# Performance work log

Hardware: AMD Instinct MI355X
Metric: run time of the kernel (lower is better)

## Reference

```python
import jax, jax.numpy as jnp
import numpy as np

N = 1_000_000   # active voxels
CIN = 32
COUT = 64
K = 9           # 3x3 kernel offsets (rulebook size)
EPS = 1e-5


def setup_inputs() -> dict:
    key = jax.random.key(0)
    ks = jax.random.split(key, 6)
    x = jax.random.normal(ks[0], (N, CIN), dtype=jnp.float32)
    # rulebook: neighbor index per (voxel, kernel offset); stride=1 so same coord set
    nbr = jax.random.randint(ks[1], (N, K), 0, N, dtype=jnp.int32)
    W1 = jax.random.normal(ks[2], (K, CIN, COUT), dtype=jnp.float32) * (1.0 / np.sqrt(K * CIN))
    W2 = jax.random.normal(ks[3], (K, COUT, COUT), dtype=jnp.float32) * (1.0 / np.sqrt(K * COUT))
    Wd = jax.random.normal(ks[4], (CIN, COUT), dtype=jnp.float32) * (1.0 / np.sqrt(CIN))
    g1 = jnp.ones((COUT,), jnp.float32); b1 = jnp.zeros((COUT,), jnp.float32)
    g2 = jnp.ones((COUT,), jnp.float32); b2 = jnp.zeros((COUT,), jnp.float32)
    gd = jnp.ones((COUT,), jnp.float32); bd = jnp.zeros((COUT,), jnp.float32)
    return {"x": x, "W1": W1, "g1": g1, "b1": b1, "W2": W2, "g2": g2, "b2": b2,
            "Wd": Wd, "gd": gd, "bd": bd, "nbr": nbr}


def _sparse_conv(x, nbr, W):
    # gather-GEMM-scatter; loop over the fixed K=9 kernel offsets to avoid
    # materializing the full [N, K, Cin] gathered tensor
    out = jnp.zeros((x.shape[0], W.shape[-1]), dtype=x.dtype)
    for k in range(W.shape[0]):
        out = out + jnp.take(x, nbr[:, k], axis=0) @ W[k]
    return out


def _bn(x, gamma, beta):
    # BatchNorm1d over the voxel dimension (training-mode batch statistics)
    mu = jnp.mean(x, axis=0)
    var = jnp.var(x, axis=0)
    return gamma * (x - mu) * jax.lax.rsqrt(var + EPS) + beta


def reference(x, W1, g1, b1, W2, g2, b2, Wd, gd, bd, nbr):
    # downsample branch (1x1 conv -> BN, no relu) since in_ch != out_ch
    identity = _bn(x @ Wd, gd, bd)
    # conv1: SparseConv3x3 -> BN -> ReLU
    out = jax.nn.relu(_bn(_sparse_conv(x, nbr, W1), g1, b1))
    # conv2: SparseConv3x3 -> BN (no relu)
    out = _bn(_sparse_conv(out, nbr, W2), g2, b2)
    # residual add + final ReLU
    return jax.nn.relu(out + identity)
```

## Files before the change

### kernel.cpp

```cpp
#include <hip/hip_runtime.h>
#include <hip/hip_bf16.h>

#define NV 1000000
#define CI 32
#define CO 64
#define KK 9
#define NG (NV / 16)
#define EPSV 1e-5f

typedef __bf16 bf16x8 __attribute__((ext_vector_type(8)));
typedef float  f32x4  __attribute__((ext_vector_type(4)));

__device__ __forceinline__ f32x4 mfma16(bf16x8 a, bf16x8 b, f32x4 c) {
    return __builtin_amdgcn_mfma_f32_16x16x32_bf16(a, b, c, 0, 0, 0);
}

__device__ __forceinline__ float xredseg(float v) {
    v += __shfl_xor(v, 16, 64);
    v += __shfl_xor(v, 32, 64);
    return v;
}

__global__ void k_prep_w(const float* __restrict__ W1, const float* __restrict__ W2,
                         const float* __restrict__ Wd,
                         __bf16* __restrict__ W1T, __bf16* __restrict__ W2T,
                         __bf16* __restrict__ WdT) {
    int i = blockIdx.x * blockDim.x + threadIdx.x;
    const int n1 = KK * CO * CI;
    const int n2 = KK * CO * CO;
    const int nd = CO * CI;
    if (i < n1) {
        int k = i / (CO * CI), r = i % (CO * CI), co = r / CI, ci = r % CI;
        W1T[i] = (__bf16)W1[(k * CI + ci) * CO + co];
    } else if (i < n1 + n2) {
        int j = i - n1;
        int k = j / (CO * CO), r = j % (CO * CO), co = r / CO, ci = r % CO;
        W2T[j] = (__bf16)W2[(k * CO + ci) * CO + co];
    } else if (i < n1 + n2 + nd) {
        int j = i - n1 - n2;
        int co = j / CI, ci = j % CI;
        WdT[j] = (__bf16)Wd[ci * CO + co];
    }
}

__global__ void k_prep_x(const float* __restrict__ x, __bf16* __restrict__ xb) {
    int i = blockIdx.x * blockDim.x + threadIdx.x;
    const float4* px = (const float4*)x + 2 * (size_t)i;
    float4 u = px[0], v = px[1];
    bf16x8 o;
    o[0] = (__bf16)u.x; o[1] = (__bf16)u.y; o[2] = (__bf16)u.z; o[3] = (__bf16)u.w;
    o[4] = (__bf16)v.x; o[5] = (__bf16)v.y; o[6] = (__bf16)v.z; o[7] = (__bf16)v.w;
    *((bf16x8*)xb + i) = o;
}

__global__ __launch_bounds__(256, 2) void k_conv1(
    const __bf16* __restrict__ xb, const int* __restrict__ nbr,
    const __bf16* __restrict__ W1T, const __bf16* __restrict__ WdT,
    __bf16* __restrict__ y1b, float* __restrict__ stats) {
    __shared__ __align__(16) char w1smem[KK * CO * CI * 2];

    const int lane = threadIdx.x & 63;
    const int w    = threadIdx.x >> 6;
    const int r    = lane & 15;
    const int seg  = lane >> 4;
    const int sseg = seg ^ ((r >> 1) & 3);

#pragma unroll
    for (int j = 0; j < 9; j++) {
        int c    = j * 256 + threadIdx.x;
        int segc = c & 3;
        int rc   = (c >> 2) & 15;
        int csrc = (c & ~3) | (segc ^ ((rc >> 1) & 3));
        const __bf16* srcp = W1T + (size_t)csrc * 8;
        __builtin_amdgcn_global_load_lds(
            (const __attribute__((address_space(1))) void*)srcp,
            (__attribute__((address_space(3))) void*)(w1smem + j * 4096 + w * 1024),
            16, 0, 0);
    }
    __syncthreads();

    bf16x8 wd[4];
#pragma unroll
    for (int t = 0; t < 4; t++)
        wd[t] = *(const bf16x8*)(WdT + (size_t)(t * 16 + r) * CI + seg * 8);

    float ps1[4] = {0.f,0.f,0.f,0.f}, pq1[4] = {0.f,0.f,0.f,0.f};
    float psd[4] = {0.f,0.f,0.f,0.f}, pqd[4] = {0.f,0.f,0.f,0.f};

    const int slot   = blockIdx.x * 4 + w;
    const int stride = gridDim.x * 4;
    const f32x4 z = {0.f, 0.f, 0.f, 0.f};

    auto loadIdx = [&](int (&idx)[KK], int tile) {
        const int* nb = nbr + (size_t)(tile * 16 + r) * KK;
#pragma unroll
        for (int k = 0; k < KK; k++) idx[k] = nb[k];
    };
    auto gather9 = [&](bf16x8 (&g)[KK], const int (&idx)[KK]) {
#pragma unroll
        for (int k = 0; k < KK; k++)
            g[k] = *(const bf16x8*)(xb + (size_t)idx[k] * CI + seg * 8);
    };
    auto loadAd = [&](int tile) {
        return *(const bf16x8*)(xb + (size_t)(tile * 16 + r) * CI + seg * 8);
    };
    auto compute = [&](int tile, const bf16x8 (&g)[KK], bf16x8 ad) {
        int w1off = 0;
        asm volatile("" : "+v"(w1off));
        const __bf16* wb = (const __bf16*)w1smem + w1off;

        f32x4 acc[4]  = {z, z, z, z};
        f32x4 accd[4] = {z, z, z, z};
#pragma unroll
        for (int t = 0; t < 4; t++) accd[t] = mfma16(ad, wd[t], accd[t]);
#pragma unroll
        for (int k = 0; k < KK; k++) {
#pragma unroll
            for (int t = 0; t < 4; t++) {
                bf16x8 b = *(const bf16x8*)(wb + k * 2048 + t * 512 + r * 32 + sseg * 8);
                acc[t] = mfma16(g[k], b, acc[t]);
            }
        }

        const int vb = tile * 16;
#pragma unroll
        for (int t = 0; t < 4; t++) {
#pragma unroll
            for (int rr = 0; rr < 4; rr++) {
                float val = acc[t][rr];
                int row = vb + seg * 4 + rr;
                __builtin_nontemporal_store((__bf16)val, &y1b[(size_t)row * CO + t * 16 + r]);
                ps1[t] += val; pq1[t] += val * val;
                float dv = accd[t][rr];
                psd[t] += dv; pqd[t] += dv * dv;
            }
        }
    };

    int idx0[KK], idx1[KK];
    bf16x8 g0[KK], g1[KK];
    bf16x8 ad0, ad1;

    int it = slot;
    loadIdx(idx0, it);
    gather9(g0, idx0); ad0 = loadAd(it);
    int itn = it + stride;
    bool have = (itn < NG);
    if (have) loadIdx(idx1, itn);

    while (true) {
        if (have) {
            gather9(g1, idx1); ad1 = loadAd(itn);
            int it2 = itn + stride;
            if (it2 < NG) loadIdx(idx0, it2);
        }
        compute(it, g0, ad0);
        if (!have) break;
        it = itn; itn = it + stride; have = (itn < NG);

        if (have) {
            gather9(g0, idx0); ad0 = loadAd(itn);
            int it2 = itn + stride;
            if (it2 < NG) loadIdx(idx1, it2);
        }
        compute(it, g1, ad1);
        if (!have) break;
        it = itn; itn = it + stride; have = (itn < NG);
    }

#pragma unroll
    for (int t = 0; t < 4; t++) {
        ps1[t] = xredseg(ps1[t]); pq1[t] = xredseg(pq1[t]);
        psd[t] = xredseg(psd[t]); pqd[t] = xredseg(pqd[t]);
    }
    if (lane < 16) {
#pragma unroll
        for (int t = 0; t < 4; t++) {
            atomicAdd(&stats[0 * 64 + t * 16 + lane], ps1[t]);
            atomicAdd(&stats[1 * 64 + t * 16 + lane], pq1[t]);
            atomicAdd(&stats[2 * 64 + t * 16 + lane], psd[t]);
            atomicAdd(&stats[3 * 64 + t * 16 + lane], pqd[t]);
        }
    }
}

#define TILE_B (16 * KK * 128)

__global__ __launch_bounds__(128, 2) void k_conv2(
    const __bf16* __restrict__ h1b, const int* __restrict__ nbr,
    const __bf16* __restrict__ W2T, const float* __restrict__ g1,
    const float* __restrict__ b1,
    float* __restrict__ y2, float* __restrict__ stats) {
    __shared__ __align__(16) char smem[2][TILE_B];

    const int lane = threadIdx.x & 63;
    const int w    = threadIdx.x >> 6;
    const int r    = lane & 15;
    const int seg  = lane >> 4;
    const int p    = lane & 7;

    bf16x8 w2[KK][2][2];
#pragma unroll
    for (int k = 0; k < KK; k++)
#pragma unroll
        for (int t2 = 0; t2 < 2; t2++)
#pragma unroll
            for (int s = 0; s < 2; s++) {
                int co = w * 32 + t2 * 16 + r;
                int ci = s * 32 + seg * 8;
                w2[k][t2][s] = *(const bf16x8*)(W2T + ((size_t)(k * CO + co)) * CO + ci);
            }

    float scP[8], shP[8];
#pragma unroll
    for (int j = 0; j < 8; j++) {
        int c0 = p * 8 + j;
        float mu  = stats[c0] * (1.0f / NV);
        float var = stats[64 + c0] * (1.0f / NV) - mu * mu;
        float s   = g1[c0] * rsqrtf(var + EPSV);
        scP[j] = s; shP[j] = b1[c0] - mu * s;
    }

    int ri[9], dstoff[9];
#pragma unroll
    for (int s = 0; s < 9; s++) {
        int c = w * 576 + s * 64 + lane;
        int rIdx = c >> 3;
        int i = (rIdx * 57) >> 9;
        ri[s] = rIdx;
        dstoff[s] = rIdx * 128 + ((p ^ (i & 7)) * 16);
    }

    auto loadIdx = [&](int (&ix)[9], int tile) {
        const int* nb = nbr + (size_t)tile * (16 * KK);
#pragma unroll
        for (int s = 0; s < 9; s++) ix[s] = nb[ri[s]];
    };
    auto loadDat = [&](f32x4 (&d)[9], const int (&ix)[9]) {
#pragma unroll
        for (int s = 0; s < 9; s++)
            d[s] = *(const f32x4*)(h1b + (size_t)ix[s] * CO + p * 8);
    };
    auto xform = [&](char* tb, const f32x4 (&d)[9]) {
#pragma unroll
        for (int s = 0; s < 9; s++) {
            union { f32x4 f; bf16x8 b; } u; u.f = d[s];
            bf16x8 o;
#pragma unroll
            for (int j = 0; j < 8; j++)
                o[j] = (__bf16)fmaxf((float)u.b[j] * scP[j] + shP[j], 0.f);
            *(bf16x8*)(tb + dstoff[s]) = o;
        }
    };

    float ps[2] = {0.f, 0.f}, pq[2] = {0.f, 0.f};
    const f32x4 z = {0.f, 0.f, 0.f, 0.f};
    const int sw = r & 7;
    const int G = gridDim.x;

    int idxN[9]; f32x4 dat[9];
    int it = blockIdx.x;
    loadIdx(idxN, it);
    loadDat(dat, idxN);
    { int t1 = it + G;     loadIdx(idxN, t1 < NG ? t1 : NG - 1); }
    xform(smem[0], dat);
    loadDat(dat, idxN);
    { int t2 = it + 2 * G; loadIdx(idxN, t2 < NG ? t2 : NG - 1); }
    __syncthreads();
    int cur = 0;

    for (; it < NG; it += G) {
        const __bf16* base = (const __bf16*)smem[cur];
        f32x4 acc[2] = {z, z};
#pragma unroll
        for (int k = 0; k < KK; k++) {
            const __bf16* rp = base + (size_t)(r * KK + k) * 64;
            bf16x8 a0 = *(const bf16x8*)(rp + ((seg ^ sw) * 8));
            bf16x8 a1 = *(const bf16x8*)(rp + (((4 + seg) ^ sw) * 8));
            acc[0] = mfma16(a0, w2[k][0][0], acc[0]);
            acc[0] = mfma16(a1, w2[k][0][1], acc[0]);
            acc[1] = mfma16(a0, w2[k][1][0], acc[1]);
            acc[1] = mfma16(a1, w2[k][1][1], acc[1]);
        }

        const int vb = it * 16;
#pragma unroll
        for (int t2 = 0; t2 < 2; t2++) {
#pragma unroll
            for (int rr = 0; rr < 4; rr++) {
                float val = acc[t2][rr];
                int row = vb + seg * 4 + rr;
                int c = w * 32 + t2 * 16 + r;
                __builtin_nontemporal_store(val, &y2[(size_t)row * CO + c]);
                ps[t2] += val; pq[t2] += val * val;
            }
        }

        int nx = it + G;
        if (nx < NG) {
            xform(smem[cur ^ 1], dat);
            loadDat(dat, idxN);
            { int t3 = it + 3 * G; loadIdx(idxN, t3 < NG ? t3 : NG - 1); }
            __syncthreads();
            cur ^= 1;
        }
    }

#pragma unroll
    for (int t2 = 0; t2 < 2; t2++) { ps[t2] = xredseg(ps[t2]); pq[t2] = xredseg(pq[t2]); }
    if (lane < 16) {
#pragma unroll
        for (int t2 = 0; t2 < 2; t2++) {
            atomicAdd(&stats[4 * 64 + w * 32 + t2 * 16 + lane], ps[t2]);
            atomicAdd(&stats[5 * 64 + w * 32 + t2 * 16 + lane], pq[t2]);
        }
    }
}

__global__ __launch_bounds__(256, 2) void k_final(
    const __bf16* __restrict__ xb, const __bf16* __restrict__ WdT,
    float* __restrict__ out, const float* __restrict__ stats,
    const float* __restrict__ g2, const float* __restrict__ b2,
    const float* __restrict__ gd, const float* __restrict__ bd) {
    __shared__ float s2[CO], sh2[CO], sdv[CO], shd[CO];
    int t = threadIdx.x;
    if (t < CO) {
        float mu2  = stats[4 * 64 + t] * (1.0f / NV);
        float var2 = stats[5 * 64 + t] * (1.0f / NV) - mu2 * mu2;
        float s = g2[t] * rsqrtf(var2 + EPSV);
        s2[t] = s; sh2[t] = b2[t] - mu2 * s;
        float mud  = stats[2 * 64 + t] * (1.0f / NV);
        float vard = stats[3 * 64 + t] * (1.0f / NV) - mud * mud;
        float sd = gd[t] * rsqrtf(vard + EPSV);
        sdv[t] = sd; shd[t] = bd[t] - mud * sd;
    }
    __syncthreads();

    const int lane = threadIdx.x & 63;
    const int w    = threadIdx.x >> 6;
    const int r    = lane & 15;
    const int seg  = lane >> 4;

    bf16x8 wd[4];
#pragma unroll
    for (int t4 = 0; t4 < 4; t4++)
        wd[t4] = *(const bf16x8*)(WdT + (size_t)(t4 * 16 + r) * CI + seg * 8);

    const int slot = blockIdx.x * 4 + w;
    const int nslots = gridDim.x * 4;
    const f32x4 z = {0.f, 0.f, 0.f, 0.f};

    for (int gid = slot; gid < NG; gid += nslots) {
        const int vb = gid * 16;
        const int v  = vb + r;
        bf16x8 ad = *(const bf16x8*)(xb + (size_t)v * CI + seg * 8);
        f32x4 accd[4] = {z, z, z, z};
#pragma unroll
        for (int t4 = 0; t4 < 4; t4++) accd[t4] = mfma16(ad, wd[t4], accd[t4]);
#pragma unroll
        for (int t4 = 0; t4 < 4; t4++) {
#pragma unroll
            for (int rr = 0; rr < 4; rr++) {
                int row = vb + seg * 4 + rr;
                int c = t4 * 16 + r;
                size_t o = (size_t)row * CO + c;
                float y2v = out[o];
                float res = s2[c] * y2v + sh2[c] + sdv[c] * accd[t4][rr] + shd[c];
                out[o] = fmaxf(res, 0.f);
            }
        }
    }
}

extern "C" void kernel_launch(void* const* d_in, const int* in_sizes, int n_in,
                              void* d_out, int out_size, void* d_ws, size_t ws_size,
                              hipStream_t stream) {
    const float* x  = (const float*)d_in[0];
    const float* W1 = (const float*)d_in[1];
    const float* g1 = (const float*)d_in[2];
    const float* b1 = (const float*)d_in[3];
    const float* W2 = (const float*)d_in[4];
    const float* g2 = (const float*)d_in[5];
    const float* b2 = (const float*)d_in[6];
    const float* Wd = (const float*)d_in[7];
    const float* gd = (const float*)d_in[8];
    const float* bd = (const float*)d_in[9];
    const int*  nbr = (const int*)d_in[10];

    char* ws = (char*)d_ws;
    __bf16* xb  = (__bf16*)ws;
    __bf16* y1b = (__bf16*)(ws + 64000000);
    __bf16* W1T = (__bf16*)(ws + 192000000);
    __bf16* W2T = W1T + KK * CO * CI;
    __bf16* WdT = W2T + KK * CO * CO;
    float* stats = (float*)(ws + 192000000 + 2 * (KK*CO*CI + KK*CO*CO + CO*CI));

    hipMemsetAsync(stats, 0, 6 * 64 * sizeof(float), stream);

    int nprep = KK*CO*CI + KK*CO*CO + CO*CI;
    k_prep_w<<<(nprep + 255) / 256, 256, 0, stream>>>(W1, W2, Wd, W1T, W2T, WdT);
    k_prep_x<<<(NV * CI / 8) / 256, 256, 0, stream>>>(x, xb);
    k_conv1<<<768, 256, 0, stream>>>(xb, nbr, W1T, WdT, y1b, stats);
    k_conv2<<<1024, 128, 0, stream>>>(y1b, nbr, W2T, g1, b1, (float*)d_out, stats);
    k_final<<<1024, 256, 0, stream>>>(xb, WdT, (float*)d_out, stats, g2, b2, gd, bd);
}
```

Before: 601.5 us.

## Stage conv outputs through LDS for wide stores and keep conv2 output in bf16

conv1 now writes its bf16 tile into a swizzled per-wave LDS buffer and then stores 16-byte vectors, instead of scattering 2-byte nontemporal stores. When the workspace is large enough, conv2 does the same and keeps its output as a bf16 intermediate, so the final kernel reads half the bytes and writes the fp32 output with nontemporal stores. This cuts write and readback traffic for the intermediates. It adds LDS usage and an extra rounding of the pre-BN conv2 output to bf16, and the bf16 path depends on the workspace size.

```diff
diff --git a/kernel.cpp b/kernel.cpp
--- a/kernel.cpp
+++ b/kernel.cpp
@@ -9,6 +9,7 @@
 #define EPSV 1e-5f
 
 typedef __bf16 bf16x8 __attribute__((ext_vector_type(8)));
+typedef __bf16 bf16x4 __attribute__((ext_vector_type(4)));
 typedef float  f32x4  __attribute__((ext_vector_type(4)));
 
 __device__ __forceinline__ f32x4 mfma16(bf16x8 a, bf16x8 b, f32x4 c) {
@@ -58,6 +59,7 @@
     const __bf16* __restrict__ W1T, const __bf16* __restrict__ WdT,
     __bf16* __restrict__ y1b, float* __restrict__ stats) {
     __shared__ __align__(16) char w1smem[KK * CO * CI * 2];
+    __shared__ __align__(16) char ystage[4][2048];
 
     const int lane = threadIdx.x & 63;
     const int w    = threadIdx.x >> 6;
@@ -123,17 +125,28 @@
         }
 
         const int vb = tile * 16;
+        char* yst = ystage[w];
 #pragma unroll
         for (int t = 0; t < 4; t++) {
 #pragma unroll
             for (int rr = 0; rr < 4; rr++) {
                 float val = acc[t][rr];
-                int row = vb + seg * 4 + rr;
-                __builtin_nontemporal_store((__bf16)val, &y1b[(size_t)row * CO + t * 16 + r]);
                 ps1[t] += val; pq1[t] += val * val;
                 float dv = accd[t][rr];
                 psd[t] += dv; pqd[t] += dv * dv;
-            }
+                int row = seg * 4 + rr;
+                int byte = row * 128 + ((t * 32 + 2 * r) ^ ((row & 7) << 4));
+                *(__bf16*)(yst + byte) = (__bf16)val;
+            }
+        }
+#pragma unroll
+        for (int q = 0; q < 2; q++) {
+            int c    = lane * 2 + q;
+            int row  = c >> 3;
+            int part = c & 7;
+            bf16x8 v = *(const bf16x8*)(yst + row * 128 + ((part ^ (row & 7)) << 4));
+            __builtin_nontemporal_store(
+                v, (bf16x8*)(y1b + (size_t)vb * CO + (size_t)c * 8));
         }
     };
 
@@ -186,12 +199,15 @@
 
 #define TILE_B (16 * KK * 128)
 
+template <bool BF16OUT>
 __global__ __launch_bounds__(128, 2) void k_conv2(
     const __bf16* __restrict__ h1b, const int* __restrict__ nbr,
     const __bf16* __restrict__ W2T, const float* __restrict__ g1,
     const float* __restrict__ b1,
-    float* __restrict__ y2, float* __restrict__ stats) {
+    __bf16* __restrict__ y2b, float* __restrict__ y2f,
+    float* __restrict__ stats) {
     __shared__ __align__(16) char smem[2][TILE_B];
+    __shared__ __align__(16) char ystage2[2][1024];
 
     const int lane = threadIdx.x & 63;
     const int w    = threadIdx.x >> 6;
@@ -284,15 +300,37 @@
         }
 
         const int vb = it * 16;
-#pragma unroll
-        for (int t2 = 0; t2 < 2; t2++) {
-#pragma unroll
-            for (int rr = 0; rr < 4; rr++) {
-                float val = acc[t2][rr];
-                int row = vb + seg * 4 + rr;
-                int c = w * 32 + t2 * 16 + r;
-                __builtin_nontemporal_store(val, &y2[(size_t)row * CO + c]);
-                ps[t2] += val; pq[t2] += val * val;
+        if constexpr (BF16OUT) {
+            char* yst = ystage2[w];
+#pragma unroll
+            for (int t2 = 0; t2 < 2; t2++) {
+#pragma unroll
+                for (int rr = 0; rr < 4; rr++) {
+                    float val = acc[t2][rr];
+                    ps[t2] += val; pq[t2] += val * val;
+                    int row = seg * 4 + rr;
+                    int byte = row * 64 + ((t2 * 32 + 2 * r) ^ ((row >> 2) << 4));
+                    *(__bf16*)(yst + byte) = (__bf16)val;
+                }
+            }
+            {
+                int row  = lane >> 2;
+                int part = lane & 3;
+                bf16x8 v = *(const bf16x8*)(yst + row * 64 + ((part ^ (row >> 2)) << 4));
+                __builtin_nontemporal_store(
+                    v, (bf16x8*)(y2b + (size_t)(vb + row) * CO + w * 32 + part * 8));
+            }
+        } else {
+#pragma unroll
+            for (int t2 = 0; t2 < 2; t2++) {
+#pragma unroll
+                for (int rr = 0; rr < 4; rr++) {
+                    float val = acc[t2][rr];
+                    int row = vb + seg * 4 + rr;
+                    int c = w * 32 + t2 * 16 + r;
+                    __builtin_nontemporal_store(val, &y2f[(size_t)row * CO + c]);
+                    ps[t2] += val; pq[t2] += val * val;
+                }
             }
         }
 
@@ -317,8 +355,10 @@
     }
 }
 
+template <bool BF16IN>
 __global__ __launch_bounds__(256, 2) void k_final(
     const __bf16* __restrict__ xb, const __bf16* __restrict__ WdT,
+    const __bf16* __restrict__ y2b,
     float* __restrict__ out, const float* __restrict__ stats,
     const float* __restrict__ g2, const float* __restrict__ b2,
     const float* __restrict__ gd, const float* __restrict__ bd) {
@@ -364,9 +404,11 @@
                 int row = vb + seg * 4 + rr;
                 int c = t4 * 16 + r;
                 size_t o = (size_t)row * CO + c;
-                float y2v = out[o];
+                float y2v;
+                if constexpr (BF16IN) y2v = (float)y2b[o];
+                else                  y2v = out[o];
                 float res = s2[c] * y2v + sh2[c] + sdv[c] * accd[t4][rr] + shd[c];
-                out[o] = fmaxf(res, 0.f);
+                __builtin_nontemporal_store(fmaxf(res, 0.f), &out[o]);
             }
         }
     }
@@ -394,6 +436,9 @@
     __bf16* W2T = W1T + KK * CO * CI;
     __bf16* WdT = W2T + KK * CO * CO;
     float* stats = (float*)(ws + 192000000 + 2 * (KK*CO*CI + KK*CO*CO + CO*CI));
+    size_t y2off = ((192000000 + 2 * (KK*CO*CI + KK*CO*CO + CO*CI) + 6*64*4) + 255) & ~(size_t)255;
+    __bf16* y2b = (__bf16*)(ws + y2off);
+    bool bf16y2 = (ws_size >= y2off + (size_t)NV * CO * 2 + 256);
 
     hipMemsetAsync(stats, 0, 6 * 64 * sizeof(float), stream);
 
@@ -401,6 +446,15 @@
     k_prep_w<<<(nprep + 255) / 256, 256, 0, stream>>>(W1, W2, Wd, W1T, W2T, WdT);
     k_prep_x<<<(NV * CI / 8) / 256, 256, 0, stream>>>(x, xb);
     k_conv1<<<768, 256, 0, stream>>>(xb, nbr, W1T, WdT, y1b, stats);
-    k_conv2<<<1024, 128, 0, stream>>>(y1b, nbr, W2T, g1, b1, (float*)d_out, stats);
-    k_final<<<1024, 256, 0, stream>>>(xb, WdT, (float*)d_out, stats, g2, b2, gd, bd);
-}
+    if (bf16y2) {
+        k_conv2<true><<<1024, 128, 0, stream>>>(y1b, nbr, W2T, g1, b1,
+                                                y2b, nullptr, stats);
+        k_final<true><<<1024, 256, 0, stream>>>(xb, WdT, y2b, (float*)d_out, stats,
+                                                g2, b2, gd, bd);
+    } else {
+        k_conv2<false><<<1024, 128, 0, stream>>>(y1b, nbr, W2T, g1, b1,
+                                                 nullptr, (float*)d_out, stats);
+        k_final<false><<<1024, 256, 0, stream>>>(xb, WdT, nullptr, (float*)d_out, stats,
+                                                 g2, b2, gd, bd);
+    }
+}
```

Result: no change. 591.3 us (-1.7%).
